# Kernel tuning notes

Hardware: AMD Instinct MI355X
Metric: run time of the kernel (lower is better)

The kernel has to match this reference:

```python
import jax, jax.numpy as jnp
import numpy as np

DIM = 1024
NUM_HEADS = 16
HEAD_DIM = DIM // NUM_HEADS
SCALE = 1.0 / float(np.sqrt(HEAD_DIM))


def setup_inputs() -> dict:
    key = jax.random.key(0)
    ks = jax.random.split(key, 5)
    B, S = 2, 2048
    x = jax.random.normal(ks[0], (B, S, DIM), dtype=jnp.float32)
    qkv_w = jax.random.normal(ks[1], (3 * DIM, DIM), dtype=jnp.float32) * (1.0 / np.sqrt(DIM))
    qkv_b = jax.random.normal(ks[2], (3 * DIM,), dtype=jnp.float32) * 0.02
    proj_w = jax.random.normal(ks[3], (DIM, DIM), dtype=jnp.float32) * (1.0 / np.sqrt(DIM))
    proj_b = jax.random.normal(ks[4], (DIM,), dtype=jnp.float32) * 0.02
    return {"x": x, "qkv_w": qkv_w, "qkv_b": qkv_b, "proj_w": proj_w, "proj_b": proj_b}


def reference(x, qkv_w, qkv_b, proj_w, proj_b):
    B, S, _ = x.shape
    # qkv projection: (B,S,3*DIM) -> (3, B, H, S, Dh)
    qkv = x @ qkv_w.T + qkv_b
    qkv = qkv.reshape(B, S, 3, NUM_HEADS, HEAD_DIM).transpose(2, 0, 3, 1, 4)
    q, k, v = qkv[0], qkv[1], qkv[2]
    # scaled dot-product attention (full score matrix, as in the original)
    scores = jnp.einsum('bhqd,bhkd->bhqk', q, k) * SCALE
    attn = jax.nn.softmax(scores, axis=-1)
    out = jnp.einsum('bhqk,bhkd->bhqd', attn, v)  # (B,H,S,Dh)
    out = out.transpose(0, 2, 1, 3).reshape(B, S, DIM)
    return out @ proj_w.T + proj_b
```

## Files before the change

### kernel.cpp

```cpp
#include <hip/hip_runtime.h>

#define DIM_ 1024
#define NH_ 16
#define HD_ 64
#define B_ 2
#define S_ 2048
#define M_ (B_ * S_)
#define NQKV_ (3 * DIM_)

typedef __attribute__((ext_vector_type(8))) __bf16 bf16x8;
typedef __attribute__((ext_vector_type(4))) __bf16 bf16x4;
typedef __attribute__((ext_vector_type(4))) float f32x4;

__device__ __forceinline__ void gl_lds16(const void* g, void* l) {
  __builtin_amdgcn_global_load_lds(
      (__attribute__((address_space(1))) void*)const_cast<void*>(g),
      (__attribute__((address_space(3))) void*)l, 16, 0, 0);
}

__global__ __launch_bounds__(256) void cast_f32_bf16(const float* __restrict__ in,
                                                     __bf16* __restrict__ out, int n4) {
  int i = blockIdx.x * 256 + threadIdx.x;
  int stride = gridDim.x * 256;
  for (; i < n4; i += stride) {
    float4 v = ((const float4*)in)[i];
    bf16x4 o;
    o[0] = (__bf16)v.x; o[1] = (__bf16)v.y; o[2] = (__bf16)v.z; o[3] = (__bf16)v.w;
    ((bf16x4*)out)[i] = o;
  }
}

template <int MODE>
__global__ __launch_bounds__(256) void gemm_bt(const __bf16* __restrict__ A,
                                               const __bf16* __restrict__ Bw,
                                               const float* __restrict__ bias,
                                               __bf16* __restrict__ Qp, __bf16* __restrict__ Kp,
                                               __bf16* __restrict__ Vp, float* __restrict__ Cout) {
  constexpr int KD = 1024;
  __shared__ __bf16 As[128 * 32];
  __shared__ __bf16 Bs[128 * 32];
  const int tid = threadIdx.x;
  const int lane = tid & 63;
  const int wave = tid >> 6;
  const int quad = lane >> 4;
  const int r16 = lane & 15;
  const int wm = wave >> 1;
  const int wn = wave & 1;
  const int m0 = blockIdx.y * 128;
  const int n0 = blockIdx.x * 128;

  const f32x4 fz = {0.f, 0.f, 0.f, 0.f};
  f32x4 acc[4][4];
#pragma unroll
  for (int i = 0; i < 4; ++i)
#pragma unroll
    for (int j = 0; j < 4; ++j) acc[i][j] = fz;

  const int c0 = tid, c1 = tid + 256;
  const __bf16* ga0 = A + (size_t)(m0 + (c0 >> 2)) * KD + (c0 & 3) * 8;
  const __bf16* ga1 = A + (size_t)(m0 + (c1 >> 2)) * KD + (c1 & 3) * 8;
  const __bf16* gb0 = Bw + (size_t)(n0 + (c0 >> 2)) * KD + (c0 & 3) * 8;
  const __bf16* gb1 = Bw + (size_t)(n0 + (c1 >> 2)) * KD + (c1 & 3) * 8;
  __bf16* la0 = &As[c0 * 8];
  __bf16* la1 = &As[c1 * 8];
  __bf16* lb0 = &Bs[c0 * 8];
  __bf16* lb1 = &Bs[c1 * 8];

  const int abase = (wm * 64 + r16) * 32 + quad * 8;
  const int bbase = (wn * 64 + r16) * 32 + quad * 8;

  for (int kt = 0; kt < KD / 32; ++kt) {
    __syncthreads();
    gl_lds16(ga0, la0);
    gl_lds16(ga1, la1);
    gl_lds16(gb0, lb0);
    gl_lds16(gb1, lb1);
    ga0 += 32; ga1 += 32; gb0 += 32; gb1 += 32;
    __syncthreads();

    bf16x8 af[4], bfr[4];
#pragma unroll
    for (int mt = 0; mt < 4; ++mt) af[mt] = *(const bf16x8*)&As[abase + mt * 16 * 32];
#pragma unroll
    for (int nt = 0; nt < 4; ++nt) bfr[nt] = *(const bf16x8*)&Bs[bbase + nt * 16 * 32];
#pragma unroll
    for (int mt = 0; mt < 4; ++mt)
#pragma unroll
      for (int nt = 0; nt < 4; ++nt)
        acc[mt][nt] = __builtin_amdgcn_mfma_f32_16x16x32_bf16(af[mt], bfr[nt], acc[mt][nt], 0, 0, 0);
  }

  if (MODE == 0) {
#pragma unroll
    for (int nt = 0; nt < 4; ++nt) {
      const int n = n0 + wn * 64 + nt * 16 + r16;
      const int sel = n >> 10;
      const int h = (n >> 6) & 15;
      const int dh = n & 63;
      const float bs = bias[n];
      __bf16* dst = (sel == 0) ? Qp : ((sel == 1) ? Kp : Vp);
      const float mul = (sel == 0) ? 0.18033688011112042f : 1.0f;
#pragma unroll
      for (int mt = 0; mt < 4; ++mt) {
#pragma unroll
        for (int r = 0; r < 4; ++r) {
          const int m = m0 + wm * 64 + mt * 16 + quad * 4 + r;
          const int b = m >> 11;
          const int s = m & 2047;
          dst[((size_t)((b * NH_ + h) * S_ + s)) * HD_ + dh] = (__bf16)((acc[mt][nt][r] + bs) * mul);
        }
      }
    }
  } else {
#pragma unroll
    for (int nt = 0; nt < 4; ++nt) {
      const int n = n0 + wn * 64 + nt * 16 + r16;
      const float bs = bias[n];
#pragma unroll
      for (int mt = 0; mt < 4; ++mt) {
#pragma unroll
        for (int r = 0; r < 4; ++r) {
          const int m = m0 + wm * 64 + mt * 16 + quad * 4 + r;
          Cout[(size_t)m * DIM_ + n] = acc[mt][nt][r] + bs;
        }
      }
    }
  }
}

__global__ __launch_bounds__(256) void transpose_v(const __bf16* __restrict__ V,
                                                   __bf16* __restrict__ Vt) {
  __shared__ __bf16 t[64][65];
  const int tid = threadIdx.x;
  const int bh = blockIdx.y;
  const int s0 = blockIdx.x * 64;
#pragma unroll
  for (int i = 0; i < 16; ++i) {
    int idx = tid + i * 256;
    int r = idx >> 6, c = idx & 63;
    t[r][c] = V[((size_t)bh * S_ + s0 + r) * HD_ + c];
  }
  __syncthreads();
#pragma unroll
  for (int i = 0; i < 16; ++i) {
    int idx = tid + i * 256;
    int r = idx >> 6, c = idx & 63;
    int src = (c & 32) | (((c >> 2) & 1) << 4) | (((c >> 3) & 3) << 2) | (c & 3);
    Vt[((size_t)bh * HD_ + r) * S_ + s0 + c] = t[src][r];
  }
}

__global__ __launch_bounds__(256) void attn(const __bf16* __restrict__ Qp,
                                            const __bf16* __restrict__ Kp,
                                            const __bf16* __restrict__ Vtp,
                                            __bf16* __restrict__ ctx) {
  __shared__ __bf16 Ks[128 * 64];
  __shared__ __bf16 Vs[64 * 128];
  const int tid = threadIdx.x;
  const int lane = tid & 63;
  const int wave = tid >> 6;
  const int quad = lane >> 4;
  const int r16 = lane & 15;
  const int bh = blockIdx.y;
  const int q0 = blockIdx.x * 64;
  const int qrow = q0 + wave * 16 + r16;

  const __bf16* qb = Qp + ((size_t)bh * S_ + qrow) * HD_;
  const bf16x8 qf0 = *(const bf16x8*)(qb + quad * 8);
  const bf16x8 qf1 = *(const bf16x8*)(qb + 32 + quad * 8);

  const f32x4 fz = {0.f, 0.f, 0.f, 0.f};
  f32x4 o[4];
#pragma unroll
  for (int d = 0; d < 4; ++d) o[d] = fz;
  float lsum = 0.f;

  const __bf16* gk[4];
  const __bf16* gv[4];
  __bf16 *lk[4], *lv[4];
#pragma unroll
  for (int i = 0; i < 4; ++i) {
    int c = tid + i * 256;
    int kr = c >> 3, kc = c & 7;
    gk[i] = Kp + ((size_t)bh * S_ + kr) * HD_ + ((kc ^ (kr & 7)) * 8);
    lk[i] = &Ks[c * 8];
    int vr = c >> 4, vc = c & 15;
    gv[i] = Vtp + ((size_t)bh * HD_ + vr) * S_ + ((vc ^ (vr & 15)) * 8);
    lv[i] = &Vs[c * 8];
  }

  for (int kt = 0; kt < S_ / 128; ++kt) {
    __syncthreads();
#pragma unroll
    for (int i = 0; i < 4; ++i) { gl_lds16(gk[i], lk[i]); gk[i] += 128 * HD_; }
#pragma unroll
    for (int i = 0; i < 4; ++i) { gl_lds16(gv[i], lv[i]); gv[i] += 128; }
    __syncthreads();

    f32x4 sa[8];
#pragma unroll
    for (int mt = 0; mt < 8; ++mt) {
      const int row = mt * 16 + r16;
      bf16x8 k0 = *(const bf16x8*)&Ks[row * 64 + ((quad ^ (row & 7)) * 8)];
      bf16x8 k1 = *(const bf16x8*)&Ks[row * 64 + (((4 + quad) ^ (row & 7)) * 8)];
      f32x4 t = fz;
      t = __builtin_amdgcn_mfma_f32_16x16x32_bf16(k0, qf0, t, 0, 0, 0);
      t = __builtin_amdgcn_mfma_f32_16x16x32_bf16(k1, qf1, t, 0, 0, 0);
      sa[mt] = t;
    }

    bf16x8 pf[4];
#pragma unroll
    for (int ks = 0; ks < 4; ++ks)
#pragma unroll
      for (int r = 0; r < 4; ++r) {
        float p0 = __builtin_amdgcn_exp2f(sa[2 * ks][r]);
        float p1 = __builtin_amdgcn_exp2f(sa[2 * ks + 1][r]);
        lsum += p0 + p1;
        pf[ks][r] = (__bf16)p0;
        pf[ks][4 + r] = (__bf16)p1;
      }

#pragma unroll
    for (int ks = 0; ks < 4; ++ks)
#pragma unroll
      for (int dt = 0; dt < 4; ++dt) {
        const int row = dt * 16 + r16;
        bf16x8 va = *(const bf16x8*)&Vs[row * 128 + (((4 * ks + quad) ^ (row & 15)) * 8)];
        o[dt] = __builtin_amdgcn_mfma_f32_16x16x32_bf16(va, pf[ks], o[dt], 0, 0, 0);
      }
  }

  lsum += __shfl_xor(lsum, 16);
  lsum += __shfl_xor(lsum, 32);
  const float inv = 1.0f / lsum;
  const int b = bh >> 4, h = bh & 15;
  const int s = q0 + wave * 16 + r16;
#pragma unroll
  for (int dt = 0; dt < 4; ++dt) {
    bf16x4 ov;
#pragma unroll
    for (int r = 0; r < 4; ++r) ov[r] = (__bf16)(o[dt][r] * inv);
    *(bf16x4*)&ctx[((size_t)(b * S_ + s)) * DIM_ + h * 64 + dt * 16 + quad * 4] = ov;
  }
}

extern "C" void kernel_launch(void* const* d_in, const int* in_sizes, int n_in, void* d_out,
                              int out_size, void* d_ws, size_t ws_size, hipStream_t stream) {
  const float* x = (const float*)d_in[0];
  const float* qkv_w = (const float*)d_in[1];
  const float* qkv_b = (const float*)d_in[2];
  const float* proj_w = (const float*)d_in[3];
  const float* proj_b = (const float*)d_in[4];
  float* out = (float*)d_out;

  char* ws = (char*)d_ws;
  __bf16* Xb = (__bf16*)(ws);
  __bf16* Wb = (__bf16*)(ws + 8388608);
  __bf16* Pb = (__bf16*)(ws + 14680064);
  __bf16* Qp = (__bf16*)(ws + 16777216);
  __bf16* Kp = (__bf16*)(ws + 25165824);
  __bf16* Vp = (__bf16*)(ws + 33554432);
  __bf16* Vt = (__bf16*)(ws + 41943040);
  __bf16* Cx = (__bf16*)(ws + 50331648);

  cast_f32_bf16<<<4096, 256, 0, stream>>>(x, Xb, M_ * DIM_ / 4);
  cast_f32_bf16<<<3072, 256, 0, stream>>>(qkv_w, Wb, NQKV_ * DIM_ / 4);
  cast_f32_bf16<<<1024, 256, 0, stream>>>(proj_w, Pb, DIM_ * DIM_ / 4);

  gemm_bt<0><<<dim3(NQKV_ / 128, M_ / 128), 256, 0, stream>>>(Xb, Wb, qkv_b, Qp, Kp, Vp, nullptr);
  transpose_v<<<dim3(S_ / 64, 32), 256, 0, stream>>>(Vp, Vt);
  attn<<<dim3(S_ / 64, 32), 256, 0, stream>>>(Qp, Kp, Vt, Cx);
  gemm_bt<1><<<dim3(DIM_ / 128, M_ / 128), 256, 0, stream>>>(Cx, Pb, proj_b, nullptr, nullptr,
                                                             nullptr, out);
}
```

Before: 197.8 us.

## Fuse casts, write V transposed from QKV GEMM, deepen K tile, double attention rows

Merges the three cast kernels into one launch. The QKV GEMM epilogue now writes V straight into the permuted transposed layout, so the separate transpose kernel goes away. The GEMM K-step grows from 32 to 64 with an XOR-swizzled LDS layout, halving the number of barrier pairs. The attention kernel handles 128 query rows per block (two 16-row groups per wave), so each K/V tile loaded into LDS is reused twice, at the cost of more registers and half as many blocks.

```diff
diff --git a/kernel.cpp b/kernel.cpp
--- a/kernel.cpp
+++ b/kernel.cpp
@@ -18,15 +18,28 @@
       (__attribute__((address_space(3))) void*)l, 16, 0, 0);
 }
 
-__global__ __launch_bounds__(256) void cast_f32_bf16(const float* __restrict__ in,
-                                                     __bf16* __restrict__ out, int n4) {
+#define N4_X 1048576
+#define N4_W1 786432
+#define N4_W2 262144
+__global__ __launch_bounds__(256) void cast_all(const float* __restrict__ x,
+                                                const float* __restrict__ w1,
+                                                const float* __restrict__ w2,
+                                                __bf16* __restrict__ xb,
+                                                __bf16* __restrict__ w1b,
+                                                __bf16* __restrict__ w2b) {
   int i = blockIdx.x * 256 + threadIdx.x;
-  int stride = gridDim.x * 256;
-  for (; i < n4; i += stride) {
-    float4 v = ((const float4*)in)[i];
+  const int stride = gridDim.x * 256;
+  for (; i < N4_X + N4_W1 + N4_W2; i += stride) {
+    const float4* src;
+    bf16x4* dst;
+    int j;
+    if (i < N4_X) { src = (const float4*)x; dst = (bf16x4*)xb; j = i; }
+    else if (i < N4_X + N4_W1) { src = (const float4*)w1; dst = (bf16x4*)w1b; j = i - N4_X; }
+    else { src = (const float4*)w2; dst = (bf16x4*)w2b; j = i - (N4_X + N4_W1); }
+    float4 v = src[j];
     bf16x4 o;
     o[0] = (__bf16)v.x; o[1] = (__bf16)v.y; o[2] = (__bf16)v.z; o[3] = (__bf16)v.w;
-    ((bf16x4*)out)[i] = o;
+    dst[j] = o;
   }
 }
 
@@ -35,10 +48,10 @@
                                                const __bf16* __restrict__ Bw,
                                                const float* __restrict__ bias,
                                                __bf16* __restrict__ Qp, __bf16* __restrict__ Kp,
-                                               __bf16* __restrict__ Vp, float* __restrict__ Cout) {
+                                               __bf16* __restrict__ Vt, float* __restrict__ Cout) {
   constexpr int KD = 1024;
-  __shared__ __bf16 As[128 * 32];
-  __shared__ __bf16 Bs[128 * 32];
+  __shared__ __bf16 As[128 * 64];
+  __shared__ __bf16 Bs[128 * 64];
   const int tid = threadIdx.x;
   const int lane = tid & 63;
   const int wave = tid >> 6;
@@ -56,38 +69,48 @@
 #pragma unroll
     for (int j = 0; j < 4; ++j) acc[i][j] = fz;
 
-  const int c0 = tid, c1 = tid + 256;
-  const __bf16* ga0 = A + (size_t)(m0 + (c0 >> 2)) * KD + (c0 & 3) * 8;
-  const __bf16* ga1 = A + (size_t)(m0 + (c1 >> 2)) * KD + (c1 & 3) * 8;
-  const __bf16* gb0 = Bw + (size_t)(n0 + (c0 >> 2)) * KD + (c0 & 3) * 8;
-  const __bf16* gb1 = Bw + (size_t)(n0 + (c1 >> 2)) * KD + (c1 & 3) * 8;
-  __bf16* la0 = &As[c0 * 8];
-  __bf16* la1 = &As[c1 * 8];
-  __bf16* lb0 = &Bs[c0 * 8];
-  __bf16* lb1 = &Bs[c1 * 8];
-
-  const int abase = (wm * 64 + r16) * 32 + quad * 8;
-  const int bbase = (wn * 64 + r16) * 32 + quad * 8;
-
-  for (int kt = 0; kt < KD / 32; ++kt) {
+  const __bf16* ga[4];
+  const __bf16* gb[4];
+  __bf16 *la[4], *lb[4];
+#pragma unroll
+  for (int i = 0; i < 4; ++i) {
+    const int c = tid + i * 256;
+    const int r = c >> 3, cc = c & 7;
+    const int col = ((cc ^ (r & 7)) * 8);
+    ga[i] = A + (size_t)(m0 + r) * KD + col;
+    gb[i] = Bw + (size_t)(n0 + r) * KD + col;
+    la[i] = &As[c * 8];
+    lb[i] = &Bs[c * 8];
+  }
+
+  for (int kt = 0; kt < KD / 64; ++kt) {
     __syncthreads();
-    gl_lds16(ga0, la0);
-    gl_lds16(ga1, la1);
-    gl_lds16(gb0, lb0);
-    gl_lds16(gb1, lb1);
-    ga0 += 32; ga1 += 32; gb0 += 32; gb1 += 32;
+#pragma unroll
+    for (int i = 0; i < 4; ++i) {
+      gl_lds16(ga[i], la[i]); ga[i] += 64;
+      gl_lds16(gb[i], lb[i]); gb[i] += 64;
+    }
     __syncthreads();
 
-    bf16x8 af[4], bfr[4];
-#pragma unroll
-    for (int mt = 0; mt < 4; ++mt) af[mt] = *(const bf16x8*)&As[abase + mt * 16 * 32];
-#pragma unroll
-    for (int nt = 0; nt < 4; ++nt) bfr[nt] = *(const bf16x8*)&Bs[bbase + nt * 16 * 32];
-#pragma unroll
-    for (int mt = 0; mt < 4; ++mt)
+    bf16x8 af[2][4], bfr[2][4];
+#pragma unroll
+    for (int sub = 0; sub < 2; ++sub) {
+      const int ch = ((sub * 4 + quad) ^ (r16 & 7)) * 8;
+#pragma unroll
+      for (int mt = 0; mt < 4; ++mt)
+        af[sub][mt] = *(const bf16x8*)&As[(wm * 64 + mt * 16 + r16) * 64 + ch];
 #pragma unroll
       for (int nt = 0; nt < 4; ++nt)
-        acc[mt][nt] = __builtin_amdgcn_mfma_f32_16x16x32_bf16(af[mt], bfr[nt], acc[mt][nt], 0, 0, 0);
+        bfr[sub][nt] = *(const bf16x8*)&Bs[(wn * 64 + nt * 16 + r16) * 64 + ch];
+    }
+#pragma unroll
+    for (int sub = 0; sub < 2; ++sub)
+#pragma unroll
+      for (int mt = 0; mt < 4; ++mt)
+#pragma unroll
+        for (int nt = 0; nt < 4; ++nt)
+          acc[mt][nt] =
+              __builtin_amdgcn_mfma_f32_16x16x32_bf16(af[sub][mt], bfr[sub][nt], acc[mt][nt], 0, 0, 0);
   }
 
   if (MODE == 0) {
@@ -98,16 +121,31 @@
       const int h = (n >> 6) & 15;
       const int dh = n & 63;
       const float bs = bias[n];
-      __bf16* dst = (sel == 0) ? Qp : ((sel == 1) ? Kp : Vp);
-      const float mul = (sel == 0) ? 0.18033688011112042f : 1.0f;
-#pragma unroll
-      for (int mt = 0; mt < 4; ++mt) {
-#pragma unroll
-        for (int r = 0; r < 4; ++r) {
-          const int m = m0 + wm * 64 + mt * 16 + quad * 4 + r;
+      if (sel == 2) {
+#pragma unroll
+        for (int mt = 0; mt < 4; ++mt) {
+          const int m = m0 + wm * 64 + mt * 16 + quad * 4;
           const int b = m >> 11;
           const int s = m & 2047;
-          dst[((size_t)((b * NH_ + h) * S_ + s)) * HD_ + dh] = (__bf16)((acc[mt][nt][r] + bs) * mul);
+          const int slot = (s & ~31) | (((s >> 2) & 3) << 3) | (((s >> 4) & 1) << 2);
+          bf16x4 ov;
+#pragma unroll
+          for (int r = 0; r < 4; ++r) ov[r] = (__bf16)(acc[mt][nt][r] + bs);
+          *(bf16x4*)&Vt[((size_t)((b * NH_ + h) * HD_ + dh)) * S_ + slot] = ov;
+        }
+      } else {
+        __bf16* dst = (sel == 0) ? Qp : Kp;
+        const float mul = (sel == 0) ? 0.18033688011112042f : 1.0f;
+#pragma unroll
+        for (int mt = 0; mt < 4; ++mt) {
+#pragma unroll
+          for (int r = 0; r < 4; ++r) {
+            const int m = m0 + wm * 64 + mt * 16 + quad * 4 + r;
+            const int b = m >> 11;
+            const int s = m & 2047;
+            dst[((size_t)((b * NH_ + h) * S_ + s)) * HD_ + dh] =
+                (__bf16)((acc[mt][nt][r] + bs) * mul);
+          }
         }
       }
     }
@@ -125,28 +163,6 @@
         }
       }
     }
-  }
-}
-
-__global__ __launch_bounds__(256) void transpose_v(const __bf16* __restrict__ V,
-                                                   __bf16* __restrict__ Vt) {
-  __shared__ __bf16 t[64][65];
-  const int tid = threadIdx.x;
-  const int bh = blockIdx.y;
-  const int s0 = blockIdx.x * 64;
-#pragma unroll
-  for (int i = 0; i < 16; ++i) {
-    int idx = tid + i * 256;
-    int r = idx >> 6, c = idx & 63;
-    t[r][c] = V[((size_t)bh * S_ + s0 + r) * HD_ + c];
-  }
-  __syncthreads();
-#pragma unroll
-  for (int i = 0; i < 16; ++i) {
-    int idx = tid + i * 256;
-    int r = idx >> 6, c = idx & 63;
-    int src = (c & 32) | (((c >> 2) & 1) << 4) | (((c >> 3) & 3) << 2) | (c & 3);
-    Vt[((size_t)bh * HD_ + r) * S_ + s0 + c] = t[src][r];
   }
 }
 
@@ -162,18 +178,23 @@
   const int quad = lane >> 4;
   const int r16 = lane & 15;
   const int bh = blockIdx.y;
-  const int q0 = blockIdx.x * 64;
-  const int qrow = q0 + wave * 16 + r16;
-
-  const __bf16* qb = Qp + ((size_t)bh * S_ + qrow) * HD_;
-  const bf16x8 qf0 = *(const bf16x8*)(qb + quad * 8);
-  const bf16x8 qf1 = *(const bf16x8*)(qb + 32 + quad * 8);
+  const int q0 = blockIdx.x * 128;
+
+  bf16x8 qf[2][2];
+#pragma unroll
+  for (int g = 0; g < 2; ++g) {
+    const __bf16* qb = Qp + ((size_t)bh * S_ + q0 + wave * 32 + g * 16 + r16) * HD_;
+    qf[g][0] = *(const bf16x8*)(qb + quad * 8);
+    qf[g][1] = *(const bf16x8*)(qb + 32 + quad * 8);
+  }
 
   const f32x4 fz = {0.f, 0.f, 0.f, 0.f};
-  f32x4 o[4];
-#pragma unroll
-  for (int d = 0; d < 4; ++d) o[d] = fz;
-  float lsum = 0.f;
+  f32x4 o[2][4];
+  float lsum[2] = {0.f, 0.f};
+#pragma unroll
+  for (int g = 0; g < 2; ++g)
+#pragma unroll
+    for (int d = 0; d < 4; ++d) o[g][d] = fz;
 
   const __bf16* gk[4];
   const __bf16* gv[4];
@@ -197,29 +218,34 @@
     for (int i = 0; i < 4; ++i) { gl_lds16(gv[i], lv[i]); gv[i] += 128; }
     __syncthreads();
 
-    f32x4 sa[8];
+    f32x4 sa[2][8];
 #pragma unroll
     for (int mt = 0; mt < 8; ++mt) {
       const int row = mt * 16 + r16;
       bf16x8 k0 = *(const bf16x8*)&Ks[row * 64 + ((quad ^ (row & 7)) * 8)];
       bf16x8 k1 = *(const bf16x8*)&Ks[row * 64 + (((4 + quad) ^ (row & 7)) * 8)];
-      f32x4 t = fz;
-      t = __builtin_amdgcn_mfma_f32_16x16x32_bf16(k0, qf0, t, 0, 0, 0);
-      t = __builtin_amdgcn_mfma_f32_16x16x32_bf16(k1, qf1, t, 0, 0, 0);
-      sa[mt] = t;
-    }
-
-    bf16x8 pf[4];
-#pragma unroll
-    for (int ks = 0; ks < 4; ++ks)
-#pragma unroll
-      for (int r = 0; r < 4; ++r) {
-        float p0 = __builtin_amdgcn_exp2f(sa[2 * ks][r]);
-        float p1 = __builtin_amdgcn_exp2f(sa[2 * ks + 1][r]);
-        lsum += p0 + p1;
-        pf[ks][r] = (__bf16)p0;
-        pf[ks][4 + r] = (__bf16)p1;
+#pragma unroll
+      for (int g = 0; g < 2; ++g) {
+        f32x4 t = fz;
+        t = __builtin_amdgcn_mfma_f32_16x16x32_bf16(k0, qf[g][0], t, 0, 0, 0);
+        t = __builtin_amdgcn_mfma_f32_16x16x32_bf16(k1, qf[g][1], t, 0, 0, 0);
+        sa[g][mt] = t;
       }
+    }
+
+    bf16x8 pf[2][4];
+#pragma unroll
+    for (int g = 0; g < 2; ++g)
+#pragma unroll
+      for (int ks = 0; ks < 4; ++ks)
+#pragma unroll
+        for (int r = 0; r < 4; ++r) {
+          float p0 = __builtin_amdgcn_exp2f(sa[g][2 * ks][r]);
+          float p1 = __builtin_amdgcn_exp2f(sa[g][2 * ks + 1][r]);
+          lsum[g] += p0 + p1;
+          pf[g][ks][r] = (__bf16)p0;
+          pf[g][ks][4 + r] = (__bf16)p1;
+        }
 
 #pragma unroll
     for (int ks = 0; ks < 4; ++ks)
@@ -227,21 +253,27 @@
       for (int dt = 0; dt < 4; ++dt) {
         const int row = dt * 16 + r16;
         bf16x8 va = *(const bf16x8*)&Vs[row * 128 + (((4 * ks + quad) ^ (row & 15)) * 8)];
-        o[dt] = __builtin_amdgcn_mfma_f32_16x16x32_bf16(va, pf[ks], o[dt], 0, 0, 0);
+#pragma unroll
+        for (int g = 0; g < 2; ++g)
+          o[g][dt] = __builtin_amdgcn_mfma_f32_16x16x32_bf16(va, pf[g][ks], o[g][dt], 0, 0, 0);
       }
   }
 
-  lsum += __shfl_xor(lsum, 16);
-  lsum += __shfl_xor(lsum, 32);
-  const float inv = 1.0f / lsum;
   const int b = bh >> 4, h = bh & 15;
-  const int s = q0 + wave * 16 + r16;
-#pragma unroll
-  for (int dt = 0; dt < 4; ++dt) {
-    bf16x4 ov;
-#pragma unroll
-    for (int r = 0; r < 4; ++r) ov[r] = (__bf16)(o[dt][r] * inv);
-    *(bf16x4*)&ctx[((size_t)(b * S_ + s)) * DIM_ + h * 64 + dt * 16 + quad * 4] = ov;
+#pragma unroll
+  for (int g = 0; g < 2; ++g) {
+    float l = lsum[g];
+    l += __shfl_xor(l, 16);
+    l += __shfl_xor(l, 32);
+    const float inv = 1.0f / l;
+    const int s = q0 + wave * 32 + g * 16 + r16;
+#pragma unroll
+    for (int dt = 0; dt < 4; ++dt) {
+      bf16x4 ov;
+#pragma unroll
+      for (int r = 0; r < 4; ++r) ov[r] = (__bf16)(o[g][dt][r] * inv);
+      *(bf16x4*)&ctx[((size_t)(b * S_ + s)) * DIM_ + h * 64 + dt * 16 + quad * 4] = ov;
+    }
   }
 }
 
@@ -260,17 +292,12 @@
   __bf16* Pb = (__bf16*)(ws + 14680064);
   __bf16* Qp = (__bf16*)(ws + 16777216);
   __bf16* Kp = (__bf16*)(ws + 25165824);
-  __bf16* Vp = (__bf16*)(ws + 33554432);
-  __bf16* Vt = (__bf16*)(ws + 41943040);
-  __bf16* Cx = (__bf16*)(ws + 50331648);
-
-  cast_f32_bf16<<<4096, 256, 0, stream>>>(x, Xb, M_ * DIM_ / 4);
-  cast_f32_bf16<<<3072, 256, 0, stream>>>(qkv_w, Wb, NQKV_ * DIM_ / 4);
-  cast_f32_bf16<<<1024, 256, 0, stream>>>(proj_w, Pb, DIM_ * DIM_ / 4);
-
-  gemm_bt<0><<<dim3(NQKV_ / 128, M_ / 128), 256, 0, stream>>>(Xb, Wb, qkv_b, Qp, Kp, Vp, nullptr);
-  transpose_v<<<dim3(S_ / 64, 32), 256, 0, stream>>>(Vp, Vt);
-  attn<<<dim3(S_ / 64, 32), 256, 0, stream>>>(Qp, Kp, Vt, Cx);
+  __bf16* Vt = (__bf16*)(ws + 33554432);
+  __bf16* Cx = (__bf16*)(ws + 41943040);
+
+  cast_all<<<2048, 256, 0, stream>>>(x, qkv_w, proj_w, Xb, Wb, Pb);
+  gemm_bt<0><<<dim3(NQKV_ / 128, M_ / 128), 256, 0, stream>>>(Xb, Wb, qkv_b, Qp, Kp, Vt, nullptr);
+  attn<<<dim3(S_ / 128, 32), 256, 0, stream>>>(Qp, Kp, Vt, Cx);
   gemm_bt<1><<<dim3(DIM_ / 128, M_ / 128), 256, 0, stream>>>(Cx, Pb, proj_b, nullptr, nullptr,
                                                              nullptr, out);
 }
```

After: 188.1 us. -4.9%, faster.
